# Kernel optimization log

Hardware: AMD Instinct MI355X
Metric: run time of the kernel (lower is better)

## Reference

```python
import jax, jax.numpy as jnp
import numpy as np

# DAG configuration (fixed, mirrors the networkx dG used at construction time)
B = 4096          # batch
N_INP = 4096      # genes
L0 = 512          # leaf GO terms, each mapped to G disjoint genes
G = 8             # genes per leaf term
H = 16            # module_neurons (uniform per-module hidden size)
FAN = 8           # children per internal module -> input size FAN*H = 128
L1, L2 = 64, 8    # internal level sizes; root has L2=8 children


def setup_inputs() -> dict:
    key = jax.random.key(0)
    ks = jax.random.split(key, 8)
    s = lambda *sh: 0.1
    x = jax.random.normal(ks[0], (B, N_INP), dtype=jnp.float32)
    # Gene (RestrictedLayer) effective weights: kernel*connections is one-hot,
    # so only kernel[gene_idx[m,j], j] survives -> store as [L0, G] + bias.
    Wg = jax.random.normal(ks[1], (L0, G), dtype=jnp.float32) * 0.1
    bg = jax.random.normal(ks[2], (L0, G), dtype=jnp.float32) * 0.1
    # Per-level module Dense kernels (sigmoid, no bias)
    W0 = jax.random.normal(ks[3], (L0, G, H), dtype=jnp.float32) * 0.1       # leaf terms: G -> H
    W1 = jax.random.normal(ks[4], (L1, FAN * H, H), dtype=jnp.float32) * 0.1  # 128 -> 16
    W2 = jax.random.normal(ks[5], (L2, FAN * H, H), dtype=jnp.float32) * 0.1  # 128 -> 16
    W3 = jax.random.normal(ks[6], (FAN * H, H), dtype=jnp.float32) * 0.1      # root: 128 -> 16
    Wf = jax.random.normal(ks[7], (H, 1), dtype=jnp.float32) * 0.1            # final linear, no bias
    return {"x": x, "Wg": Wg, "bg": bg, "W0": W0, "W1": W1, "W2": W2,
            "W3": W3, "Wf": Wf}


def reference(x, Wg, bg, W0, W1, W2, W3, Wf):
    b = x.shape[0]
    # Input gene layers (RestrictedLayer, linear activation):
    # leaf m owns contiguous genes [m*G, (m+1)*G) -> gather is a reshape.
    gene_out = x.reshape(b, L0, G) * Wg + bg                    # [B, L0, G]
    # Level 0 (leaf GO terms): Dense(G->H), sigmoid, no bias
    h0 = jax.nn.sigmoid(jnp.einsum('bmg,mgh->bmh', gene_out, W0))   # [B, L0, H]
    # Level 1: concat FAN children's H outputs -> Dense(FAN*H -> H), sigmoid
    h1 = jax.nn.sigmoid(jnp.einsum('bmk,mkh->bmh',
                                   h0.reshape(b, L1, FAN * H), W1))  # [B, L1, H]
    # Level 2
    h2 = jax.nn.sigmoid(jnp.einsum('bmk,mkh->bmh',
                                   h1.reshape(b, L2, FAN * H), W2))  # [B, L2, H]
    # Root 'GO:output'
    hr = jax.nn.sigmoid(h2.reshape(b, FAN * H) @ W3)                 # [B, H]
    # Final Dense(1), linear, no bias
    return hr @ Wf                                                   # [B, 1]
```

## Files before the change

### kernel.cpp

```cpp
#include <hip/hip_runtime.h>
#include <hip/hip_bf16.h>


#define TB 16
#define XSS 520
#define H0S 1032
#define H1S 136

typedef __attribute__((ext_vector_type(8))) short short8;
typedef __attribute__((ext_vector_type(4))) float floatx4;

__device__ __forceinline__ float sigf(float v) {
    return __builtin_amdgcn_rcpf(1.0f + __expf(-v));
}
__device__ __forceinline__ float bflo(unsigned int p) {
    return __builtin_bit_cast(float, p << 16);
}
__device__ __forceinline__ float bfhi(unsigned int p) {
    return __builtin_bit_cast(float, p & 0xffff0000u);
}
__device__ __forceinline__ unsigned int f2bf_u32(float f) {
    unsigned int u = __builtin_bit_cast(unsigned int, f);
    return (u + 0x7fffu + ((u >> 16) & 1u)) >> 16;
}
__device__ __forceinline__ unsigned short f2bf(float f) {
    return (unsigned short)f2bf_u32(f);
}
__device__ __forceinline__ unsigned int f2bf2(float lo, float hi) {
    return f2bf_u32(lo) | (f2bf_u32(hi) << 16);
}

__global__ __launch_bounds__(256) void k_prep(
    const float* __restrict__ W1, const float* __restrict__ W2,
    unsigned short* __restrict__ W1t, unsigned short* __restrict__ W2t)
{
    __shared__ float wl[128 * 17];
    const int mb = blockIdx.x;
    const float* src = (mb < 64) ? (W1 + (size_t)mb * 2048)
                                 : (W2 + (size_t)(mb - 64) * 2048);
    unsigned short* dst = (mb < 64) ? (W1t + (size_t)mb * 2048)
                                    : (W2t + (size_t)(mb - 64) * 2048);
    const int tid = threadIdx.x;
#pragma unroll
    for (int i = 0; i < 8; ++i) {
        const int idx = tid + i * 256;
        wl[(idx >> 4) * 17 + (idx & 15)] = src[idx];
    }
    __syncthreads();
#pragma unroll
    for (int i = 0; i < 4; ++i) {
        const int u  = tid + i * 256;
        const int h  = u >> 6;
        const int k  = (u & 63) * 2;
        ((unsigned int*)dst)[u] = f2bf2(wl[k * 17 + h], wl[(k + 1) * 17 + h]);
    }
}

__global__ __launch_bounds__(256) void k_tree(
    const float* __restrict__ x, const float* __restrict__ Wg,
    const float* __restrict__ bg, const float* __restrict__ W0,
    const unsigned short* __restrict__ W1t, const unsigned short* __restrict__ W2t,
    float* __restrict__ h2ws)
{
    __shared__ __align__(16) unsigned short xs[TB * XSS];
    __shared__ __align__(16) unsigned short h0s[TB * H0S];
    unsigned short* h1u = xs;

    const int tid  = threadIdx.x;
    const int s    = blockIdx.x & 7;
    const int b0   = (blockIdx.x >> 3) * TB;
    const int lane = tid & 63;
    const int wv   = tid >> 6;

    const float* xbase = x + (size_t)b0 * 4096 + s * 512;
    uint2 xp[8];
#pragma unroll
    for (int t = 0; t < 8; ++t) {
        const int i = tid + t * 256;
        const int r = i >> 7, c4 = i & 127;
        const float4 v = *(const float4*)(xbase + (size_t)r * 4096 + c4 * 4);
        xp[t] = make_uint2(f2bf2(v.x, v.y), f2bf2(v.z, v.w));
    }

    const int m_l = tid >> 2;
    const int hq  = tid & 3;
    const int m   = s * 64 + m_l;
    float4 w0r[8];
#pragma unroll
    for (int g = 0; g < 8; ++g)
        w0r[g] = *(const float4*)(W0 + (size_t)m * 128 + g * 16 + hq * 4);
    const float4 wg0 = *(const float4*)(Wg + m * 8);
    const float4 wg1 = *(const float4*)(Wg + m * 8 + 4);
    const float4 bg0 = *(const float4*)(bg + m * 8);
    const float4 bg1 = *(const float4*)(bg + m * 8 + 4);

    const int n = lane & 15, q = lane >> 4;
    short8 w1r[2][4];
#pragma unroll
    for (int jj = 0; jj < 2; ++jj) {
        const unsigned short* w1m =
            W1t + ((size_t)(s * 8 + wv * 2 + jj) * 16 + n) * 128 + q * 8;
#pragma unroll
        for (int ks = 0; ks < 4; ++ks)
            w1r[jj][ks] = *(const short8*)(w1m + ks * 32);
    }
    short8 w2r[4];
    if (wv == 0) {
        const unsigned short* w2m = W2t + ((size_t)s * 16 + n) * 128 + q * 8;
#pragma unroll
        for (int ks = 0; ks < 4; ++ks) w2r[ks] = *(const short8*)(w2m + ks * 32);
    }

#pragma unroll
    for (int t = 0; t < 8; ++t) {
        const int i = tid + t * 256;
        const int r = i >> 7, c4 = i & 127;
        *(uint2*)&xs[r * XSS + c4 * 4] = xp[t];
    }
    __syncthreads();

    {
        unsigned short* h0base = &h0s[m_l * 16 + hq * 4];
#pragma unroll 4
        for (int b = 0; b < TB; ++b) {
            const uint4 xv = *(const uint4*)&xs[b * XSS + m_l * 8];
            float gene[8];
            gene[0] = fmaf(bflo(xv.x), wg0.x, bg0.x);
            gene[1] = fmaf(bfhi(xv.x), wg0.y, bg0.y);
            gene[2] = fmaf(bflo(xv.y), wg0.z, bg0.z);
            gene[3] = fmaf(bfhi(xv.y), wg0.w, bg0.w);
            gene[4] = fmaf(bflo(xv.z), wg1.x, bg1.x);
            gene[5] = fmaf(bfhi(xv.z), wg1.y, bg1.y);
            gene[6] = fmaf(bflo(xv.w), wg1.z, bg1.z);
            gene[7] = fmaf(bfhi(xv.w), wg1.w, bg1.w);
            float a0 = 0.f, a1 = 0.f, a2 = 0.f, a3 = 0.f;
#pragma unroll
            for (int g = 0; g < 8; ++g) {
                a0 = fmaf(gene[g], w0r[g].x, a0);
                a1 = fmaf(gene[g], w0r[g].y, a1);
                a2 = fmaf(gene[g], w0r[g].z, a2);
                a3 = fmaf(gene[g], w0r[g].w, a3);
            }
            *(uint2*)(h0base + b * H0S) =
                make_uint2(f2bf2(sigf(a0), sigf(a1)), f2bf2(sigf(a2), sigf(a3)));
        }
    }
    __syncthreads();

    {
#pragma unroll
        for (int jj = 0; jj < 2; ++jj) {
            const int j = wv * 2 + jj;
            const unsigned short* am = &h0s[n * H0S + j * 128 + q * 8];
            floatx4 acc = {0.f, 0.f, 0.f, 0.f};
#pragma unroll
            for (int ks = 0; ks < 4; ++ks) {
                const short8 av = *(const short8*)(am + ks * 32);
                acc = __builtin_amdgcn_mfma_f32_16x16x32_bf16(av, w1r[jj][ks], acc, 0, 0, 0);
            }
#pragma unroll
            for (int r = 0; r < 4; ++r)
                h1u[(q * 4 + r) * H1S + j * 16 + n] = f2bf(sigf(acc[r]));
        }
    }
    __syncthreads();

    if (wv == 0) {
        const unsigned short* am = &h1u[n * H1S + q * 8];
        floatx4 acc = {0.f, 0.f, 0.f, 0.f};
#pragma unroll
        for (int ks = 0; ks < 4; ++ks) {
            const short8 av = *(const short8*)(am + ks * 32);
            acc = __builtin_amdgcn_mfma_f32_16x16x32_bf16(av, w2r[ks], acc, 0, 0, 0);
        }
#pragma unroll
        for (int r = 0; r < 4; ++r)
            h2ws[(size_t)(b0 + q * 4 + r) * 128 + s * 16 + n] = sigf(acc[r]);
    }
}

__global__ __launch_bounds__(128) void k_root(
    const float* __restrict__ h2ws, const float* __restrict__ W3,
    const float* __restrict__ Wf, float* __restrict__ out)
{
    __shared__ float w3s[2048];
    __shared__ float wfs[16];
    const int tid = threadIdx.x;
#pragma unroll
    for (int t = 0; t < 16; ++t) w3s[tid + t * 128] = W3[tid + t * 128];
    if (tid < 16) wfs[tid] = Wf[tid];
    __syncthreads();

    const int h = tid & 15;
    const int b = blockIdx.x * 8 + (tid >> 4);
    const float4* hp = (const float4*)(h2ws + (size_t)b * 128);
    float acc = 0.f;
#pragma unroll
    for (int k4 = 0; k4 < 32; ++k4) {
        const float4 hv = hp[k4];
        acc = fmaf(hv.x, w3s[(k4 * 4 + 0) * 16 + h], acc);
        acc = fmaf(hv.y, w3s[(k4 * 4 + 1) * 16 + h], acc);
        acc = fmaf(hv.z, w3s[(k4 * 4 + 2) * 16 + h], acc);
        acc = fmaf(hv.w, w3s[(k4 * 4 + 3) * 16 + h], acc);
    }
    float v = sigf(acc) * wfs[h];
    v += __shfl_down(v, 8, 16);
    v += __shfl_down(v, 4, 16);
    v += __shfl_down(v, 2, 16);
    v += __shfl_down(v, 1, 16);
    if (h == 0) out[b] = v;
}

extern "C" void kernel_launch(void* const* d_in, const int* in_sizes, int n_in,
                              void* d_out, int out_size, void* d_ws, size_t ws_size,
                              hipStream_t stream) {
    const float* x  = (const float*)d_in[0];
    const float* Wg = (const float*)d_in[1];
    const float* bg = (const float*)d_in[2];
    const float* W0 = (const float*)d_in[3];
    const float* W1 = (const float*)d_in[4];
    const float* W2 = (const float*)d_in[5];
    const float* W3 = (const float*)d_in[6];
    const float* Wf = (const float*)d_in[7];
    float* out = (float*)d_out;

    float* h2 = (float*)d_ws;
    unsigned short* W1t = (unsigned short*)((char*)d_ws + (size_t)2 * 1024 * 1024);
    unsigned short* W2t = W1t + (size_t)64 * 2048;

    k_prep<<<dim3(72), dim3(256), 0, stream>>>(W1, W2, W1t, W2t);
    k_tree<<<dim3((4096 / TB) * 8), dim3(256), 0, stream>>>(x, Wg, bg, W0, W1t, W2t, h2);
    k_root<<<dim3(4096 / 8), dim3(128), 0, stream>>>(h2, W3, Wf, out);
}
```

Before: 121.9 us.

## Fuse root layer into tree kernel with per-block loop over subtrees

Each block now handles 16 batch rows across all 8 level-2 subtrees in a sequential loop, keeping h2 in shared memory and computing the root and final layers in-kernel. This removes the separate root kernel launch and the global h2 round trip. The next subtree's x slice and weights are prefetched into registers during the current iteration. The cost is fewer blocks (256 of 512 threads), which limits parallelism on a large GPU, plus a serial dependency across the 8 iterations.

After: 139.1 us. 14.1% more time.

```diff
diff --git a/kernel.cpp b/kernel.cpp
--- a/kernel.cpp
+++ b/kernel.cpp
@@ -6,6 +6,7 @@
 #define XSS 520
 #define H0S 1032
 #define H1S 136
+#define H2S 132
 
 typedef __attribute__((ext_vector_type(8))) short short8;
 typedef __attribute__((ext_vector_type(4))) float floatx4;
@@ -56,159 +57,184 @@
     }
 }
 
-__global__ __launch_bounds__(256) void k_tree(
+__global__ __launch_bounds__(512, 2) void k_tree(
     const float* __restrict__ x, const float* __restrict__ Wg,
     const float* __restrict__ bg, const float* __restrict__ W0,
     const unsigned short* __restrict__ W1t, const unsigned short* __restrict__ W2t,
-    float* __restrict__ h2ws)
+    const float* __restrict__ W3, const float* __restrict__ Wf,
+    float* __restrict__ out)
 {
     __shared__ __align__(16) unsigned short xs[TB * XSS];
     __shared__ __align__(16) unsigned short h0s[TB * H0S];
-    unsigned short* h1u = xs;
+    __shared__ __align__(16) unsigned short h1u[TB * H1S];
+    __shared__ __align__(16) float h2s[TB * H2S];
+    __shared__ float w3s[2048];
+    __shared__ float wfs[16];
 
     const int tid  = threadIdx.x;
-    const int s    = blockIdx.x & 7;
-    const int b0   = (blockIdx.x >> 3) * TB;
+    const int b0   = blockIdx.x * TB;
     const int lane = tid & 63;
     const int wv   = tid >> 6;
-
-    const float* xbase = x + (size_t)b0 * 4096 + s * 512;
-    uint2 xp[8];
-#pragma unroll
-    for (int t = 0; t < 8; ++t) {
-        const int i = tid + t * 256;
-        const int r = i >> 7, c4 = i & 127;
-        const float4 v = *(const float4*)(xbase + (size_t)r * 4096 + c4 * 4);
-        xp[t] = make_uint2(f2bf2(v.x, v.y), f2bf2(v.z, v.w));
-    }
-
-    const int m_l = tid >> 2;
-    const int hq  = tid & 3;
-    const int m   = s * 64 + m_l;
-    float4 w0r[8];
+    const int half = tid >> 8;
+    const int m_l  = (tid >> 2) & 63;
+    const int hq   = tid & 3;
+    const int n    = lane & 15, q = lane >> 4;
+
+    *(float4*)&w3s[tid * 4] = *(const float4*)(W3 + tid * 4);
+    if (tid < 16) wfs[tid] = Wf[tid];
+
+    float4 xp[4];
+    {
+        const float* xb = x + (size_t)b0 * 4096;
+#pragma unroll
+        for (int t = 0; t < 4; ++t) {
+            const int i = tid + t * 512, r = i >> 7, c4 = i & 127;
+            xp[t] = *(const float4*)(xb + (size_t)r * 4096 + c4 * 4);
+        }
+    }
+    float4 w0r[8], wg0, wg1, bg0, bg1;
 #pragma unroll
     for (int g = 0; g < 8; ++g)
-        w0r[g] = *(const float4*)(W0 + (size_t)m * 128 + g * 16 + hq * 4);
-    const float4 wg0 = *(const float4*)(Wg + m * 8);
-    const float4 wg1 = *(const float4*)(Wg + m * 8 + 4);
-    const float4 bg0 = *(const float4*)(bg + m * 8);
-    const float4 bg1 = *(const float4*)(bg + m * 8 + 4);
-
-    const int n = lane & 15, q = lane >> 4;
-    short8 w1r[2][4];
-#pragma unroll
-    for (int jj = 0; jj < 2; ++jj) {
-        const unsigned short* w1m =
-            W1t + ((size_t)(s * 8 + wv * 2 + jj) * 16 + n) * 128 + q * 8;
-#pragma unroll
-        for (int ks = 0; ks < 4; ++ks)
-            w1r[jj][ks] = *(const short8*)(w1m + ks * 32);
-    }
+        w0r[g] = *(const float4*)(W0 + (size_t)m_l * 128 + g * 16 + hq * 4);
+    wg0 = *(const float4*)(Wg + m_l * 8);
+    wg1 = *(const float4*)(Wg + m_l * 8 + 4);
+    bg0 = *(const float4*)(bg + m_l * 8);
+    bg1 = *(const float4*)(bg + m_l * 8 + 4);
+
+    short8 w1r[4];
+#pragma unroll
+    for (int ks = 0; ks < 4; ++ks)
+        w1r[ks] = *(const short8*)(W1t + (size_t)wv * 2048 + n * 128 + q * 8 + ks * 32);
     short8 w2r[4];
     if (wv == 0) {
-        const unsigned short* w2m = W2t + ((size_t)s * 16 + n) * 128 + q * 8;
-#pragma unroll
-        for (int ks = 0; ks < 4; ++ks) w2r[ks] = *(const short8*)(w2m + ks * 32);
-    }
-
-#pragma unroll
-    for (int t = 0; t < 8; ++t) {
-        const int i = tid + t * 256;
-        const int r = i >> 7, c4 = i & 127;
-        *(uint2*)&xs[r * XSS + c4 * 4] = xp[t];
+#pragma unroll
+        for (int ks = 0; ks < 4; ++ks)
+            w2r[ks] = *(const short8*)(W2t + n * 128 + q * 8 + ks * 32);
+    }
+
+#pragma unroll
+    for (int t = 0; t < 4; ++t) {
+        const int i = tid + t * 512, r = i >> 7, c4 = i & 127;
+        *(uint2*)&xs[r * XSS + c4 * 4] =
+            make_uint2(f2bf2(xp[t].x, xp[t].y), f2bf2(xp[t].z, xp[t].w));
     }
     __syncthreads();
 
-    {
-        unsigned short* h0base = &h0s[m_l * 16 + hq * 4];
+#pragma unroll 1
+    for (int s = 0; s < 8; ++s) {
+        if (s < 7) {
+            const float* xb = x + (size_t)b0 * 4096 + (s + 1) * 512;
+#pragma unroll
+            for (int t = 0; t < 4; ++t) {
+                const int i = tid + t * 512, r = i >> 7, c4 = i & 127;
+                xp[t] = *(const float4*)(xb + (size_t)r * 4096 + c4 * 4);
+            }
+        }
+
+        {
+            unsigned short* h0base = &h0s[m_l * 16 + hq * 4];
 #pragma unroll 4
-        for (int b = 0; b < TB; ++b) {
-            const uint4 xv = *(const uint4*)&xs[b * XSS + m_l * 8];
-            float gene[8];
-            gene[0] = fmaf(bflo(xv.x), wg0.x, bg0.x);
-            gene[1] = fmaf(bfhi(xv.x), wg0.y, bg0.y);
-            gene[2] = fmaf(bflo(xv.y), wg0.z, bg0.z);
-            gene[3] = fmaf(bfhi(xv.y), wg0.w, bg0.w);
-            gene[4] = fmaf(bflo(xv.z), wg1.x, bg1.x);
-            gene[5] = fmaf(bfhi(xv.z), wg1.y, bg1.y);
-            gene[6] = fmaf(bflo(xv.w), wg1.z, bg1.z);
-            gene[7] = fmaf(bfhi(xv.w), wg1.w, bg1.w);
-            float a0 = 0.f, a1 = 0.f, a2 = 0.f, a3 = 0.f;
-#pragma unroll
-            for (int g = 0; g < 8; ++g) {
-                a0 = fmaf(gene[g], w0r[g].x, a0);
-                a1 = fmaf(gene[g], w0r[g].y, a1);
-                a2 = fmaf(gene[g], w0r[g].z, a2);
-                a3 = fmaf(gene[g], w0r[g].w, a3);
-            }
-            *(uint2*)(h0base + b * H0S) =
-                make_uint2(f2bf2(sigf(a0), sigf(a1)), f2bf2(sigf(a2), sigf(a3)));
-        }
-    }
-    __syncthreads();
-
-    {
-#pragma unroll
-        for (int jj = 0; jj < 2; ++jj) {
-            const int j = wv * 2 + jj;
-            const unsigned short* am = &h0s[n * H0S + j * 128 + q * 8];
+            for (int bb = 0; bb < 8; ++bb) {
+                const int b = half * 8 + bb;
+                const uint4 xv = *(const uint4*)&xs[b * XSS + m_l * 8];
+                float gene[8];
+                gene[0] = fmaf(bflo(xv.x), wg0.x, bg0.x);
+                gene[1] = fmaf(bfhi(xv.x), wg0.y, bg0.y);
+                gene[2] = fmaf(bflo(xv.y), wg0.z, bg0.z);
+                gene[3] = fmaf(bfhi(xv.y), wg0.w, bg0.w);
+                gene[4] = fmaf(bflo(xv.z), wg1.x, bg1.x);
+                gene[5] = fmaf(bfhi(xv.z), wg1.y, bg1.y);
+                gene[6] = fmaf(bflo(xv.w), wg1.z, bg1.z);
+                gene[7] = fmaf(bfhi(xv.w), wg1.w, bg1.w);
+                float a0 = 0.f, a1 = 0.f, a2 = 0.f, a3 = 0.f;
+#pragma unroll
+                for (int g = 0; g < 8; ++g) {
+                    a0 = fmaf(gene[g], w0r[g].x, a0);
+                    a1 = fmaf(gene[g], w0r[g].y, a1);
+                    a2 = fmaf(gene[g], w0r[g].z, a2);
+                    a3 = fmaf(gene[g], w0r[g].w, a3);
+                }
+                *(uint2*)(h0base + b * H0S) =
+                    make_uint2(f2bf2(sigf(a0), sigf(a1)), f2bf2(sigf(a2), sigf(a3)));
+            }
+        }
+        __syncthreads();
+
+        {
+            const unsigned short* am = &h0s[n * H0S + wv * 128 + q * 8];
             floatx4 acc = {0.f, 0.f, 0.f, 0.f};
 #pragma unroll
             for (int ks = 0; ks < 4; ++ks) {
                 const short8 av = *(const short8*)(am + ks * 32);
-                acc = __builtin_amdgcn_mfma_f32_16x16x32_bf16(av, w1r[jj][ks], acc, 0, 0, 0);
+                acc = __builtin_amdgcn_mfma_f32_16x16x32_bf16(av, w1r[ks], acc, 0, 0, 0);
             }
 #pragma unroll
             for (int r = 0; r < 4; ++r)
-                h1u[(q * 4 + r) * H1S + j * 16 + n] = f2bf(sigf(acc[r]));
-        }
-    }
-    __syncthreads();
-
-    if (wv == 0) {
-        const unsigned short* am = &h1u[n * H1S + q * 8];
-        floatx4 acc = {0.f, 0.f, 0.f, 0.f};
-#pragma unroll
-        for (int ks = 0; ks < 4; ++ks) {
-            const short8 av = *(const short8*)(am + ks * 32);
-            acc = __builtin_amdgcn_mfma_f32_16x16x32_bf16(av, w2r[ks], acc, 0, 0, 0);
-        }
-#pragma unroll
-        for (int r = 0; r < 4; ++r)
-            h2ws[(size_t)(b0 + q * 4 + r) * 128 + s * 16 + n] = sigf(acc[r]);
-    }
-}
-
-__global__ __launch_bounds__(128) void k_root(
-    const float* __restrict__ h2ws, const float* __restrict__ W3,
-    const float* __restrict__ Wf, float* __restrict__ out)
-{
-    __shared__ float w3s[2048];
-    __shared__ float wfs[16];
-    const int tid = threadIdx.x;
-#pragma unroll
-    for (int t = 0; t < 16; ++t) w3s[tid + t * 128] = W3[tid + t * 128];
-    if (tid < 16) wfs[tid] = Wf[tid];
-    __syncthreads();
-
-    const int h = tid & 15;
-    const int b = blockIdx.x * 8 + (tid >> 4);
-    const float4* hp = (const float4*)(h2ws + (size_t)b * 128);
-    float acc = 0.f;
-#pragma unroll
-    for (int k4 = 0; k4 < 32; ++k4) {
-        const float4 hv = hp[k4];
-        acc = fmaf(hv.x, w3s[(k4 * 4 + 0) * 16 + h], acc);
-        acc = fmaf(hv.y, w3s[(k4 * 4 + 1) * 16 + h], acc);
-        acc = fmaf(hv.z, w3s[(k4 * 4 + 2) * 16 + h], acc);
-        acc = fmaf(hv.w, w3s[(k4 * 4 + 3) * 16 + h], acc);
-    }
-    float v = sigf(acc) * wfs[h];
-    v += __shfl_down(v, 8, 16);
-    v += __shfl_down(v, 4, 16);
-    v += __shfl_down(v, 2, 16);
-    v += __shfl_down(v, 1, 16);
-    if (h == 0) out[b] = v;
+                h1u[(q * 4 + r) * H1S + wv * 16 + n] = f2bf(sigf(acc[r]));
+        }
+        if (s < 7) {
+#pragma unroll
+            for (int t = 0; t < 4; ++t) {
+                const int i = tid + t * 512, r = i >> 7, c4 = i & 127;
+                *(uint2*)&xs[r * XSS + c4 * 4] =
+                    make_uint2(f2bf2(xp[t].x, xp[t].y), f2bf2(xp[t].z, xp[t].w));
+            }
+            const int m2 = (s + 1) * 64 + m_l;
+#pragma unroll
+            for (int g = 0; g < 8; ++g)
+                w0r[g] = *(const float4*)(W0 + (size_t)m2 * 128 + g * 16 + hq * 4);
+            wg0 = *(const float4*)(Wg + m2 * 8);
+            wg1 = *(const float4*)(Wg + m2 * 8 + 4);
+            bg0 = *(const float4*)(bg + m2 * 8);
+            bg1 = *(const float4*)(bg + m2 * 8 + 4);
+        }
+        __syncthreads();
+
+        if (wv == 0) {
+            const unsigned short* am = &h1u[n * H1S + q * 8];
+            floatx4 acc = {0.f, 0.f, 0.f, 0.f};
+#pragma unroll
+            for (int ks = 0; ks < 4; ++ks) {
+                const short8 av = *(const short8*)(am + ks * 32);
+                acc = __builtin_amdgcn_mfma_f32_16x16x32_bf16(av, w2r[ks], acc, 0, 0, 0);
+            }
+#pragma unroll
+            for (int r = 0; r < 4; ++r)
+                h2s[(q * 4 + r) * H2S + s * 16 + n] = sigf(acc[r]);
+        }
+        if (s < 7) {
+#pragma unroll
+            for (int ks = 0; ks < 4; ++ks)
+                w1r[ks] = *(const short8*)(W1t + (size_t)((s + 1) * 8 + wv) * 2048
+                                           + n * 128 + q * 8 + ks * 32);
+            if (wv == 0) {
+#pragma unroll
+                for (int ks = 0; ks < 4; ++ks)
+                    w2r[ks] = *(const short8*)(W2t + (size_t)(s + 1) * 2048
+                                               + n * 128 + q * 8 + ks * 32);
+            }
+        }
+        __syncthreads();
+    }
+
+    if (tid < 256) {
+        const int b = tid >> 4, h = tid & 15;
+        float acc = 0.f;
+#pragma unroll
+        for (int k4 = 0; k4 < 32; ++k4) {
+            const float4 hv = *(const float4*)&h2s[b * H2S + k4 * 4];
+            acc = fmaf(hv.x, w3s[(k4 * 4 + 0) * 16 + h], acc);
+            acc = fmaf(hv.y, w3s[(k4 * 4 + 1) * 16 + h], acc);
+            acc = fmaf(hv.z, w3s[(k4 * 4 + 2) * 16 + h], acc);
+            acc = fmaf(hv.w, w3s[(k4 * 4 + 3) * 16 + h], acc);
+        }
+        float v = sigf(acc) * wfs[h];
+        v += __shfl_down(v, 8, 16);
+        v += __shfl_down(v, 4, 16);
+        v += __shfl_down(v, 2, 16);
+        v += __shfl_down(v, 1, 16);
+        if (h == 0) out[b0 + b] = v;
+    }
 }
 
 extern "C" void kernel_launch(void* const* d_in, const int* in_sizes, int n_in,
@@ -224,11 +250,10 @@
     const float* Wf = (const float*)d_in[7];
     float* out = (float*)d_out;
 
-    float* h2 = (float*)d_ws;
-    unsigned short* W1t = (unsigned short*)((char*)d_ws + (size_t)2 * 1024 * 1024);
+    unsigned short* W1t = (unsigned short*)d_ws;
     unsigned short* W2t = W1t + (size_t)64 * 2048;
 
     k_prep<<<dim3(72), dim3(256), 0, stream>>>(W1, W2, W1t, W2t);
-    k_tree<<<dim3((4096 / TB) * 8), dim3(256), 0, stream>>>(x, Wg, bg, W0, W1t, W2t, h2);
-    k_root<<<dim3(4096 / 8), dim3(128), 0, stream>>>(h2, W3, Wf, out);
-}
+    k_tree<<<dim3(4096 / TB), dim3(512), 0, stream>>>(x, Wg, bg, W0, W1t, W2t,
+                                                      W3, Wf, out);
+}
```

## Fuse root layer into tree kernel using last-block atomic counter per tile

Applied to the files above, without the earlier changes.

Removes the separate root kernel launch. Each batch tile of 16 rows is split across 8 blocks, one per sector. A per-tile atomic counter, zeroed in the prep kernel, lets the last of those 8 blocks compute the root Dense, the sigmoid and the final linear layer for its 16 rows, reading h2 from global memory after a threadfence. This cuts one kernel launch and its dependency gap. In exchange it adds an atomic, fences and extra tail work on one block per tile, and the workspace layout is rearranged to make room for the counters.

Result: slower. 333.0 us (+173.2%).

```diff
diff --git a/kernel.cpp b/kernel.cpp
--- a/kernel.cpp
+++ b/kernel.cpp
@@ -32,15 +32,17 @@
 
 __global__ __launch_bounds__(256) void k_prep(
     const float* __restrict__ W1, const float* __restrict__ W2,
-    unsigned short* __restrict__ W1t, unsigned short* __restrict__ W2t)
+    unsigned short* __restrict__ W1t, unsigned short* __restrict__ W2t,
+    int* __restrict__ cnt)
 {
     __shared__ float wl[128 * 17];
     const int mb = blockIdx.x;
+    const int tid = threadIdx.x;
+    if (mb == 0) cnt[tid] = 0;
     const float* src = (mb < 64) ? (W1 + (size_t)mb * 2048)
                                  : (W2 + (size_t)(mb - 64) * 2048);
     unsigned short* dst = (mb < 64) ? (W1t + (size_t)mb * 2048)
                                     : (W2t + (size_t)(mb - 64) * 2048);
-    const int tid = threadIdx.x;
 #pragma unroll
     for (int i = 0; i < 8; ++i) {
         const int idx = tid + i * 256;
@@ -60,15 +62,18 @@
     const float* __restrict__ x, const float* __restrict__ Wg,
     const float* __restrict__ bg, const float* __restrict__ W0,
     const unsigned short* __restrict__ W1t, const unsigned short* __restrict__ W2t,
-    float* __restrict__ h2ws)
+    const float* __restrict__ W3, const float* __restrict__ Wf,
+    float* __restrict__ h2ws, int* __restrict__ cnt, float* __restrict__ out)
 {
     __shared__ __align__(16) unsigned short xs[TB * XSS];
     __shared__ __align__(16) unsigned short h0s[TB * H0S];
+    __shared__ int lastflag;
     unsigned short* h1u = xs;
 
     const int tid  = threadIdx.x;
     const int s    = blockIdx.x & 7;
-    const int b0   = (blockIdx.x >> 3) * TB;
+    const int tile = blockIdx.x >> 3;
+    const int b0   = tile * TB;
     const int lane = tid & 63;
     const int wv   = tid >> 6;
 
@@ -177,38 +182,38 @@
         for (int r = 0; r < 4; ++r)
             h2ws[(size_t)(b0 + q * 4 + r) * 128 + s * 16 + n] = sigf(acc[r]);
     }
-}
-
-__global__ __launch_bounds__(128) void k_root(
-    const float* __restrict__ h2ws, const float* __restrict__ W3,
-    const float* __restrict__ Wf, float* __restrict__ out)
-{
-    __shared__ float w3s[2048];
-    __shared__ float wfs[16];
-    const int tid = threadIdx.x;
-#pragma unroll
-    for (int t = 0; t < 16; ++t) w3s[tid + t * 128] = W3[tid + t * 128];
-    if (tid < 16) wfs[tid] = Wf[tid];
-    __syncthreads();
-
-    const int h = tid & 15;
-    const int b = blockIdx.x * 8 + (tid >> 4);
-    const float4* hp = (const float4*)(h2ws + (size_t)b * 128);
-    float acc = 0.f;
-#pragma unroll
-    for (int k4 = 0; k4 < 32; ++k4) {
-        const float4 hv = hp[k4];
-        acc = fmaf(hv.x, w3s[(k4 * 4 + 0) * 16 + h], acc);
-        acc = fmaf(hv.y, w3s[(k4 * 4 + 1) * 16 + h], acc);
-        acc = fmaf(hv.z, w3s[(k4 * 4 + 2) * 16 + h], acc);
-        acc = fmaf(hv.w, w3s[(k4 * 4 + 3) * 16 + h], acc);
-    }
-    float v = sigf(acc) * wfs[h];
-    v += __shfl_down(v, 8, 16);
-    v += __shfl_down(v, 4, 16);
-    v += __shfl_down(v, 2, 16);
-    v += __shfl_down(v, 1, 16);
-    if (h == 0) out[b] = v;
+
+    if (wv == 0) __threadfence();
+    if (tid == 0)
+        lastflag = (atomicAdd(&cnt[tile], 1) == 7);
+    __syncthreads();
+    if (lastflag) {
+        __threadfence();
+        float* w3s = (float*)xs;
+        float* wfs = (float*)(xs + 4096);
+        *(float4*)&w3s[tid * 8]     = *(const float4*)(W3 + tid * 8);
+        *(float4*)&w3s[tid * 8 + 4] = *(const float4*)(W3 + tid * 8 + 4);
+        if (tid < 16) wfs[tid] = Wf[tid];
+        __syncthreads();
+        const int h = tid & 15;
+        const int b = b0 + (tid >> 4);
+        const float4* hp = (const float4*)(h2ws + (size_t)b * 128);
+        float acc = 0.f;
+#pragma unroll
+        for (int k4 = 0; k4 < 32; ++k4) {
+            const float4 hv = hp[k4];
+            acc = fmaf(hv.x, w3s[(k4 * 4 + 0) * 16 + h], acc);
+            acc = fmaf(hv.y, w3s[(k4 * 4 + 1) * 16 + h], acc);
+            acc = fmaf(hv.z, w3s[(k4 * 4 + 2) * 16 + h], acc);
+            acc = fmaf(hv.w, w3s[(k4 * 4 + 3) * 16 + h], acc);
+        }
+        float v = sigf(acc) * wfs[h];
+        v += __shfl_down(v, 8, 16);
+        v += __shfl_down(v, 4, 16);
+        v += __shfl_down(v, 2, 16);
+        v += __shfl_down(v, 1, 16);
+        if (h == 0) out[b] = v;
+    }
 }
 
 extern "C" void kernel_launch(void* const* d_in, const int* in_sizes, int n_in,
@@ -224,11 +229,12 @@
     const float* Wf = (const float*)d_in[7];
     float* out = (float*)d_out;
 
-    float* h2 = (float*)d_ws;
-    unsigned short* W1t = (unsigned short*)((char*)d_ws + (size_t)2 * 1024 * 1024);
+    unsigned short* W1t = (unsigned short*)d_ws;
     unsigned short* W2t = W1t + (size_t)64 * 2048;
-
-    k_prep<<<dim3(72), dim3(256), 0, stream>>>(W1, W2, W1t, W2t);
-    k_tree<<<dim3((4096 / TB) * 8), dim3(256), 0, stream>>>(x, Wg, bg, W0, W1t, W2t, h2);
-    k_root<<<dim3(4096 / 8), dim3(128), 0, stream>>>(h2, W3, Wf, out);
-}
+    int* cnt = (int*)((char*)d_ws + (size_t)288 * 1024);
+    float* h2 = (float*)((char*)d_ws + (size_t)512 * 1024);
+
+    k_prep<<<dim3(72), dim3(256), 0, stream>>>(W1, W2, W1t, W2t, cnt);
+    k_tree<<<dim3((4096 / TB) * 8), dim3(256), 0, stream>>>(
+        x, Wg, bg, W0, W1t, W2t, W3, Wf, h2, cnt, out);
+}
```

## Halve x staging LDS, XOR-swizzle h0 tile, widen root blocks

Applied to the files above, without the earlier changes.

The x staging buffer is cut to 8 rows and filled in two halves, so shared memory per block drops and occupancy can rise. The padded h0 layout is replaced by an XOR swizzle to avoid bank conflicts on the MFMA operand reads. k_root now uses 256-thread blocks with float4 weight loads. The cost is extra barriers between the two halves and more registers held for the prefetched second half.

Measured after the change: 120.6 us. No clear change (-1.1%).

```diff
diff --git a/kernel.cpp b/kernel.cpp
--- a/kernel.cpp
+++ b/kernel.cpp
@@ -3,8 +3,6 @@
 
 
 #define TB 16
-#define XSS 520
-#define H0S 1032
 #define H1S 136
 
 typedef __attribute__((ext_vector_type(8))) short short8;
@@ -62,8 +60,8 @@
     const unsigned short* __restrict__ W1t, const unsigned short* __restrict__ W2t,
     float* __restrict__ h2ws)
 {
-    __shared__ __align__(16) unsigned short xs[TB * XSS];
-    __shared__ __align__(16) unsigned short h0s[TB * H0S];
+    __shared__ __align__(16) unsigned short xs[8 * 512];
+    __shared__ __align__(16) unsigned short h0s[16 * 1024];
     unsigned short* h1u = xs;
 
     const int tid  = threadIdx.x;
@@ -73,13 +71,20 @@
     const int wv   = tid >> 6;
 
     const float* xbase = x + (size_t)b0 * 4096 + s * 512;
-    uint2 xp[8];
-#pragma unroll
-    for (int t = 0; t < 8; ++t) {
+    uint2 xpA[4], xpB[4];
+#pragma unroll
+    for (int t = 0; t < 4; ++t) {
         const int i = tid + t * 256;
         const int r = i >> 7, c4 = i & 127;
         const float4 v = *(const float4*)(xbase + (size_t)r * 4096 + c4 * 4);
-        xp[t] = make_uint2(f2bf2(v.x, v.y), f2bf2(v.z, v.w));
+        xpA[t] = make_uint2(f2bf2(v.x, v.y), f2bf2(v.z, v.w));
+    }
+#pragma unroll
+    for (int t = 0; t < 4; ++t) {
+        const int i = tid + t * 256;
+        const int r = (i >> 7) + 8, c4 = i & 127;
+        const float4 v = *(const float4*)(xbase + (size_t)r * 4096 + c4 * 4);
+        xpB[t] = make_uint2(f2bf2(v.x, v.y), f2bf2(v.z, v.w));
     }
 
     const int m_l = tid >> 2;
@@ -111,19 +116,31 @@
         for (int ks = 0; ks < 4; ++ks) w2r[ks] = *(const short8*)(w2m + ks * 32);
     }
 
-#pragma unroll
-    for (int t = 0; t < 8; ++t) {
+    char* const h0b = (char*)h0s;
+    const int h0off = m_l * 32 + hq * 8;
+#pragma unroll
+    for (int t = 0; t < 4; ++t) {
         const int i = tid + t * 256;
         const int r = i >> 7, c4 = i & 127;
-        *(uint2*)&xs[r * XSS + c4 * 4] = xp[t];
-    }
-    __syncthreads();
-
-    {
-        unsigned short* h0base = &h0s[m_l * 16 + hq * 4];
+        *(uint2*)&xs[r * 512 + c4 * 4] = xpA[t];
+    }
+    __syncthreads();
+#pragma unroll 1
+    for (int st = 0; st < 2; ++st) {
+        if (st == 1) {
+            __syncthreads();
+#pragma unroll
+            for (int t = 0; t < 4; ++t) {
+                const int i = tid + t * 256;
+                const int r = i >> 7, c4 = i & 127;
+                *(uint2*)&xs[r * 512 + c4 * 4] = xpB[t];
+            }
+            __syncthreads();
+        }
 #pragma unroll 4
-        for (int b = 0; b < TB; ++b) {
-            const uint4 xv = *(const uint4*)&xs[b * XSS + m_l * 8];
+        for (int bb = 0; bb < 8; ++bb) {
+            const int b = st * 8 + bb;
+            const uint4 xv = *(const uint4*)&xs[bb * 512 + m_l * 8];
             float gene[8];
             gene[0] = fmaf(bflo(xv.x), wg0.x, bg0.x);
             gene[1] = fmaf(bfhi(xv.x), wg0.y, bg0.y);
@@ -141,21 +158,22 @@
                 a2 = fmaf(gene[g], w0r[g].z, a2);
                 a3 = fmaf(gene[g], w0r[g].w, a3);
             }
-            *(uint2*)(h0base + b * H0S) =
+            *(uint2*)(h0b + b * 2048 + (h0off ^ ((bb & 7) << 4))) =
                 make_uint2(f2bf2(sigf(a0), sigf(a1)), f2bf2(sigf(a2), sigf(a3)));
         }
     }
     __syncthreads();
 
     {
+        const int swn = (n & 7) << 4;
 #pragma unroll
         for (int jj = 0; jj < 2; ++jj) {
             const int j = wv * 2 + jj;
-            const unsigned short* am = &h0s[n * H0S + j * 128 + q * 8];
             floatx4 acc = {0.f, 0.f, 0.f, 0.f};
 #pragma unroll
             for (int ks = 0; ks < 4; ++ks) {
-                const short8 av = *(const short8*)(am + ks * 32);
+                const short8 av = *(const short8*)(h0b + n * 2048 +
+                                   ((j * 256 + q * 16 + ks * 64) ^ swn));
                 acc = __builtin_amdgcn_mfma_f32_16x16x32_bf16(av, w1r[jj][ks], acc, 0, 0, 0);
             }
 #pragma unroll
@@ -179,20 +197,20 @@
     }
 }
 
-__global__ __launch_bounds__(128) void k_root(
+__global__ __launch_bounds__(256) void k_root(
     const float* __restrict__ h2ws, const float* __restrict__ W3,
     const float* __restrict__ Wf, float* __restrict__ out)
 {
     __shared__ float w3s[2048];
     __shared__ float wfs[16];
     const int tid = threadIdx.x;
-#pragma unroll
-    for (int t = 0; t < 16; ++t) w3s[tid + t * 128] = W3[tid + t * 128];
+    *(float4*)&w3s[tid * 8]     = *(const float4*)(W3 + tid * 8);
+    *(float4*)&w3s[tid * 8 + 4] = *(const float4*)(W3 + tid * 8 + 4);
     if (tid < 16) wfs[tid] = Wf[tid];
     __syncthreads();
 
     const int h = tid & 15;
-    const int b = blockIdx.x * 8 + (tid >> 4);
+    const int b = blockIdx.x * 16 + (tid >> 4);
     const float4* hp = (const float4*)(h2ws + (size_t)b * 128);
     float acc = 0.f;
 #pragma unroll
@@ -230,5 +248,5 @@
 
     k_prep<<<dim3(72), dim3(256), 0, stream>>>(W1, W2, W1t, W2t);
     k_tree<<<dim3((4096 / TB) * 8), dim3(256), 0, stream>>>(x, Wg, bg, W0, W1t, W2t, h2);
-    k_root<<<dim3(4096 / 8), dim3(128), 0, stream>>>(h2, W3, Wf, out);
-}
+    k_root<<<dim3(4096 / 16), dim3(256), 0, stream>>>(h2, W3, Wf, out);
+}
```
